# Performance work log

Measured on AMD Instinct MI355X. Metric: run time of the kernel, lower is better.

Reference implementation:

```python
import jax, jax.numpy as jnp
import numpy as np

N = 100_000          # entity count
NNZ = 1_600_000      # sparse support size (symmetrized)
C_IN = 16            # input channels (n_channels)
C1, C2, C3 = 32, 64, 32   # hard-coded widths in the torch module
C_EMB = 16           # target_embeddings
C_OUT = 16           # final_channels
N_OPS = 7            # equivariant basis ops used per layer
EPS = 1e-5


def _w(key, cin, cout):
    return jax.random.normal(key, (N_OPS, cin, cout), dtype=jnp.float32) / np.sqrt(N_OPS * cin)


def setup_inputs() -> dict:
    key = jax.random.key(0)
    ks = jax.random.split(key, 12)
    half = NNZ // 2
    r = jax.random.randint(ks[0], (half,), 0, N, dtype=jnp.int32)
    c = jax.random.randint(ks[1], (half,), 0, N, dtype=jnp.int32)
    # symmetrized support: entry j and entry j+half are transposes of each other
    row = jnp.concatenate([r, c])
    col = jnp.concatenate([c, r])
    perm = jnp.concatenate([jnp.arange(half, NNZ, dtype=jnp.int32),
                            jnp.arange(0, half, dtype=jnp.int32)])
    values = jax.random.normal(ks[2], (NNZ, C_IN), dtype=jnp.float32)
    return {
        "values": values, "row": row, "col": col, "perm": perm,
        "W1": _w(ks[3], C_IN, C1), "b1": jnp.zeros((C1,), jnp.float32),
        "W2": _w(ks[4], C1, C2),   "b2": jnp.zeros((C2,), jnp.float32),
        "W3": _w(ks[5], C2, C3),   "b3": jnp.zeros((C3,), jnp.float32),
        "Wp": jax.random.normal(ks[6], (C3, C_EMB), jnp.float32) / np.sqrt(C3),
        "bp": jnp.zeros((C_EMB,), jnp.float32),
        "Wl": jax.random.normal(ks[7], (C_EMB, C_OUT), jnp.float32) / np.sqrt(C_EMB),
        "bl": jnp.zeros((C_OUT,), jnp.float32),
    }


def _seg_mean(v, idx, n):
    # mean-pool nnz values into n segments
    s = jax.ops.segment_sum(v, idx, num_segments=n)
    cnt = jax.ops.segment_sum(jnp.ones((v.shape[0], 1), v.dtype), idx, num_segments=n)
    return s / jnp.maximum(cnt, 1.0)


def _eq_layer(v, row, col, perm, W, b):
    # equivariant basis restricted to the sparse support:
    # identity, transpose, row-mean broadcast (to row / to col),
    # col-mean broadcast (to row / to col), global-mean broadcast
    rm = _seg_mean(v, row, N)          # (N, cin)
    cm = _seg_mean(v, col, N)          # (N, cin)
    tm = jnp.mean(v, axis=0)           # (cin,)
    out = v @ W[0]
    out = out + v[perm] @ W[1]
    out = out + rm[row] @ W[2] + rm[col] @ W[3]
    out = out + cm[row] @ W[4] + cm[col] @ W[5]
    out = out + tm @ W[6] + b
    return out


def _rel_norm(v):
    # RelationNorm(affine=False): per-channel zero-mean unit-var over nnz
    m = jnp.mean(v, axis=0)
    var = jnp.var(v, axis=0)
    return (v - m) * jax.lax.rsqrt(var + EPS)


def reference(values, row, col, perm, W1, b1, W2, b2, W3, b3, Wp, bp, Wl, bl):
    h = _rel_norm(jax.nn.relu(_eq_layer(values, row, col, perm, W1, b1)))
    h = _rel_norm(jax.nn.relu(_eq_layer(h, row, col, perm, W2, b2)))
    h = _rel_norm(jax.nn.relu(_eq_layer(h, row, col, perm, W3, b3)))
    pooled = _seg_mean(h, row, N) @ Wp + bp   # entity pooling -> (N, C_EMB)
    out = pooled @ Wl + bl                    # final Linear head -> (N, C_OUT)
    return out
```

## Files before the change

### kernel.cpp

```cpp
#include <hip/hip_runtime.h>
#include <hip/hip_bf16.h>

constexpr int NE   = 100000;
constexpr int NZ   = 1600000;
constexpr int NZH  = NZ / 2;
constexpr int NSB  = (NE + 1023) / 1024;
constexpr float EPSV = 1e-5f;

constexpr int W1O = 0,     B1O = 3584,  W2O = 3616,  B2O = 17952, W3O = 18016,
              B3O = 32352, WPO = 32384, BPO = 32896, WLO = 32912, BLO = 33168,
              WTOT = 33184;

typedef __hip_bfloat16 bf16;
typedef __attribute__((ext_vector_type(8))) short short8v;
typedef __attribute__((ext_vector_type(4))) float f32x4;
#define MFMA_B16(A_, B_, C_) __builtin_amdgcn_mfma_f32_16x16x32_bf16((A_), (B_), (C_), 0, 0, 0)
#define PARTNER(i_) (((i_) < NZH) ? (i_) + NZH : (i_) - NZH)

__device__ __forceinline__ float4 ld_bf4(const bf16* p) {
    uint2 u = *(const uint2*)p;
    float4 r;
    r.x = __uint_as_float(u.x << 16);
    r.y = __uint_as_float(u.x & 0xffff0000u);
    r.z = __uint_as_float(u.y << 16);
    r.w = __uint_as_float(u.y & 0xffff0000u);
    return r;
}
__device__ __forceinline__ void ld_bf8v(const bf16* p, float4& lo, float4& hi) {
    uint4 u = *(const uint4*)p;
    lo.x = __uint_as_float(u.x << 16); lo.y = __uint_as_float(u.x & 0xffff0000u);
    lo.z = __uint_as_float(u.y << 16); lo.w = __uint_as_float(u.y & 0xffff0000u);
    hi.x = __uint_as_float(u.z << 16); hi.y = __uint_as_float(u.z & 0xffff0000u);
    hi.z = __uint_as_float(u.w << 16); hi.w = __uint_as_float(u.w & 0xffff0000u);
}
__device__ __forceinline__ float2 ld_bf2(const bf16* p) {
    unsigned u = *(const unsigned*)p;
    float2 r;
    r.x = __uint_as_float(u << 16);
    r.y = __uint_as_float(u & 0xffff0000u);
    return r;
}
__device__ __forceinline__ void st_bf4(bf16* p, float4 v) {
    __hip_bfloat162 lo = __float22bfloat162_rn(make_float2(v.x, v.y));
    __hip_bfloat162 hi = __float22bfloat162_rn(make_float2(v.z, v.w));
    uint2 u;
    u.x = *reinterpret_cast<unsigned int*>(&lo);
    u.y = *reinterpret_cast<unsigned int*>(&hi);
    *(uint2*)p = u;
}
__device__ __forceinline__ void st_bf8(bf16* p, float4 a, float4 b) {
    __hip_bfloat162 p0 = __float22bfloat162_rn(make_float2(a.x, a.y));
    __hip_bfloat162 p1 = __float22bfloat162_rn(make_float2(a.z, a.w));
    __hip_bfloat162 p2 = __float22bfloat162_rn(make_float2(b.x, b.y));
    __hip_bfloat162 p3 = __float22bfloat162_rn(make_float2(b.z, b.w));
    uint4 u;
    u.x = *reinterpret_cast<unsigned int*>(&p0);
    u.y = *reinterpret_cast<unsigned int*>(&p1);
    u.z = *reinterpret_cast<unsigned int*>(&p2);
    u.w = *reinterpret_cast<unsigned int*>(&p3);
    *(uint4*)p = u;
}
__device__ __forceinline__ float fin1(float v) { return (fabsf(v) < 1e30f) ? v : 0.f; }
__device__ __forceinline__ float4 fin4(float4 v) {
    v.x = fin1(v.x); v.y = fin1(v.y); v.z = fin1(v.z); v.w = fin1(v.w);
    return v;
}
__device__ __forceinline__ float4 ld_x4(const void* p, int flag, size_t q4) {
    if (flag) return ld_bf4((const bf16*)p + q4 * 4);
    return *((const float4*)p + q4);
}
__device__ __forceinline__ float4 relu4s(float4 x, float4 a, float4 b, const float* c) {
    float4 r;
    r.x = fmaxf(x.x + a.x + b.x + c[0], 0.f);
    r.y = fmaxf(x.y + a.y + b.y + c[1], 0.f);
    r.z = fmaxf(x.z + a.z + b.z + c[2], 0.f);
    r.w = fmaxf(x.w + a.w + b.w + c[3], 0.f);
    return r;
}
__device__ __forceinline__ void split8(const float* x, short8v& hi, short8v& lo) {
    #pragma unroll
    for (int i = 0; i < 8; i++) {
        bf16 h = __float2bfloat16(x[i]);
        float r = x[i] - __bfloat162float(h);
        bf16 l2 = __float2bfloat16(r);
        hi[i] = *reinterpret_cast<short*>(&h);
        lo[i] = *reinterpret_cast<short*>(&l2);
// ... 337 lines not shown
    float ae[8];
    ae[0]=c01s[o+0]+alo.x+blo.x; ae[1]=c01s[o+1]+alo.y+blo.y;
    ae[2]=c01s[o+2]+alo.z+blo.z; ae[3]=c01s[o+3]+alo.w+blo.w;
    ae[4]=c01s[o+4]+ahi.x+bhi.x; ae[5]=c01s[o+5]+ahi.y+bhi.y;
    ae[6]=c01s[o+6]+ahi.z+bhi.z; ae[7]=c01s[o+7]+ahi.w+bhi.w;
    #pragma unroll
    for (int ci = 0; ci < 16; ci++) {
        const float* w0 = W10s + ci * 32 + o;
        const float* w1 = W11s + ci * 32 + o;
        float a = xe[ci], b = xp[ci];
        #pragma unroll
        for (int u = 0; u < 8; u++) ae[u] += a * w0[u] + b * w1[u];
    }
    float4 hlo, hhi;
    hlo.x=fmaxf(ae[0],0.f); hlo.y=fmaxf(ae[1],0.f); hlo.z=fmaxf(ae[2],0.f); hlo.w=fmaxf(ae[3],0.f);
    hhi.x=fmaxf(ae[4],0.f); hhi.y=fmaxf(ae[5],0.f); hhi.z=fmaxf(ae[6],0.f); hhi.w=fmaxf(ae[7],0.f);
    st_bf4(h1 + (size_t)e * 32 + o, hlo);
    st_bf4(h1 + (size_t)e * 32 + o + 4, hhi);
    #pragma unroll
    for (int u = 0; u < 8; u++) {
        float h = fmaxf(ae[u], 0.f);
        atomicAdd(&red[o + u], h);
        atomicAdd(&red[32 + o + u], h * h);
    }
    __syncthreads();
    if (threadIdx.x < 32) {
        unsafeAtomicAdd(&Ssum[threadIdx.x], red[threadIdx.x]);
        unsafeAtomicAdd(&S2sum[threadIdx.x], red[32 + threadIdx.x]);
    }
}

template<bool STATS>
__global__ __launch_bounds__(256) void k_gsh1(const bf16* __restrict__ h1,
                                              const int* __restrict__ bucket,
                                              const int* __restrict__ off,
                                              const int* __restrict__ perm,
                                              const int* __restrict__ dflag,
                                              float* __restrict__ rawR, float* __restrict__ rawC,
                                              float* __restrict__ Ssum, float* __restrict__ S2sum) {
    __shared__ float red[64];
    if (STATS) {
        if (threadIdx.x < 64) red[threadIdx.x] = 0.f;
        __syncthreads();
    }
    int g = blockIdx.x * 64 + (threadIdx.x >> 2);
    int q = threadIdx.x & 3;
    float4 ra = {0,0,0,0}, rb = {0,0,0,0}, ca = {0,0,0,0}, cb = {0,0,0,0};
    float4 sa = {0,0,0,0}, sb = {0,0,0,0};
    int e0 = 0, e1 = 0;
    if (g < NE) { e0 = off[g]; e1 = off[g + 1]; }
    const bf16* hk = h1 + q * 8;
    if (dflag[1] == 0) {
        int idx = e0;
        for (; idx + 1 < e1; idx += 2) {
            int i0 = bucket[idx], i1 = bucket[idx + 1];
            int p0 = PARTNER(i0), p1 = PARTNER(i1);
            float4 aL, aH, bL, bH, cL, cH, dL, dH;
            ld_bf8v(hk + (size_t)i0 * 32, aL, aH);
            ld_bf8v(hk + (size_t)p0 * 32, bL, bH);
            ld_bf8v(hk + (size_t)i1 * 32, cL, cH);
            ld_bf8v(hk + (size_t)p1 * 32, dL, dH);
            ADD4(ra, aL); ADD4(rb, aH); ADD4(ca, bL); ADD4(cb, bH);
            ADD4(ra, cL); ADD4(rb, cH); ADD4(ca, dL); ADD4(cb, dH);
            if (STATS) { SQ4(sa, aL); SQ4(sb, aH); SQ4(sa, cL); SQ4(sb, cH); }
        }
        if (idx < e1) {
            int i = bucket[idx], p = PARTNER(i);
            float4 aL, aH, bL, bH;
            ld_bf8v(hk + (size_t)i * 32, aL, aH);
            ld_bf8v(hk + (size_t)p * 32, bL, bH);
            ADD4(ra, aL); ADD4(rb, aH); ADD4(ca, bL); ADD4(cb, bH);
            if (STATS) { SQ4(sa, aL); SQ4(sb, aH); }
        }
    } else {
        for (int idx = e0; idx < e1; idx++) {
            int i = bucket[idx], p = perm[i];
            float4 aL, aH, bL, bH;
            ld_bf8v(hk + (size_t)i * 32, aL, aH);
            ld_bf8v(hk + (size_t)p * 32, bL, bH);
            ADD4(ra, aL); ADD4(rb, aH); ADD4(ca, bL); ADD4(cb, bH);
            if (STATS) { SQ4(sa, aL); SQ4(sb, aH); }
        }
    }
    if (g < NE) {
        *(float4*)(rawR + (size_t)g * 64 + q * 8) = ra;
        *(float4*)(rawR + (size_t)g * 64 + q * 8 + 4) = rb;
        *(float4*)(rawC + (size_t)g * 64 + q * 8) = ca;
        *(float4*)(rawC + (size_t)g * 64 + q * 8 + 4) = cb;
    }
    if (STATS) {
        int o = q * 8;
        atomicAdd(&red[o+0], ra.x); atomicAdd(&red[o+1], ra.y);
        atomicAdd(&red[o+2], ra.z); atomicAdd(&red[o+3], ra.w);
        atomicAdd(&red[o+4], rb.x); atomicAdd(&red[o+5], rb.y);
        atomicAdd(&red[o+6], rb.z); atomicAdd(&red[o+7], rb.w);
        atomicAdd(&red[32+o+0], sa.x); atomicAdd(&red[32+o+1], sa.y);
        atomicAdd(&red[32+o+2], sa.z); atomicAdd(&red[32+o+3], sa.w);
        atomicAdd(&red[32+o+4], sb.x); atomicAdd(&red[32+o+5], sb.y);
        atomicAdd(&red[32+o+6], sb.z); atomicAdd(&red[32+o+7], sb.w);
        __syncthreads();
        if (threadIdx.x < 32) {
            unsafeAtomicAdd(&Ssum[threadIdx.x], red[threadIdx.x]);
            unsafeAtomicAdd(&S2sum[threadIdx.x], red[32 + threadIdx.x]);
        }
    }
}

template<int KH, int COUT>
__global__ void k_fold(const float* __restrict__ W, const float* __restrict__ mp,
                       const float* __restrict__ c0, bf16* __restrict__ Wfs,
                       float* __restrict__ c0f) {
    int t = blockIdx.x * 256 + threadIdx.x;
    constexpr int NT = COUT / 16;
    int f = t >> 9, r = t & 511;
    int lane = r >> 3, j = r & 7;
    int kc = f / NT, nt = f % NT;
    int kl = ((lane >> 4) << 3) + j;
    int kg = kc * 32 + kl;
    int n  = nt * 16 + (lane & 15);
    float w = 0.f;
    if (kg < 2 * KH) {
        int k  = (kg < KH) ? kg : kg - KH;
        const float* Ws = W + ((kg < KH) ? 0 : KH * COUT);
        w = Ws[k * COUT + n] * mp[64 + k];
    }
    bf16 hi = __float2bfloat16(w);
    Wfs[t] = hi;
    Wfs[4096 + t] = __float2bfloat16(w - __bfloat162float(hi));
    if (t < COUT) {
        float acc = c0[t];
        for (int k2 = 0; k2 < KH; k2++)
            acc += (-mp[k2] * mp[64 + k2]) * (W[k2 * COUT + t] + W[KH * COUT + k2 * COUT + t]);
        c0f[t] = acc;
    }
}

__global__ __launch_bounds__(256) void k_l1e(const void* __restrict__ xv,
                                             const int* __restrict__ dflag,
                                             const int* __restrict__ row,
                                             const int* __restrict__ col,
                                             const int* __restrict__ perm,
                                             const bf16* __restrict__ Wfs,
                                             const float* __restrict__ c0f,
                                             const bf16* __restrict__ A1b,
                                             const bf16* __restrict__ B1b,
                                             bf16* __restrict__ h1) {
    __shared__ __align__(16) float tr[4][16 * 36];
    __shared__ __align__(16) float c0s[32];
    if (threadIdx.x < 32) c0s[threadIdx.x] = c0f[threadIdx.x];
    const int flag = dflag[0];
    const int wv  = threadIdx.x >> 6;
    const int l   = threadIdx.x & 63;
    const int lr  = l & 15;
    const int lk  = l >> 4;
    const int tb  = lk * 4;
    float* T = tr[wv];
    short8v bh[2], bl[2];
    bh[0] = *(const short8v*)(Wfs + 0 * 512 + l * 8);
    bh[1] = *(const short8v*)(Wfs + 1 * 512 + l * 8);
    bl[0] = *(const short8v*)(Wfs + 4096 + 0 * 512 + l * 8);
    bl[1] = *(const short8v*)(Wfs + 4096 + 1 * 512 + l * 8);
    const int eE = l >> 2, q = l & 3;
    const int kq = lk & 1;
    __syncthreads();
    for (int bt = blockIdx.x; bt < NZ / 64; bt += gridDim.x) {
        const int te = bt * 64 + wv * 16;
        const int eA = te + lr;
        const int src = (lk < 2) ? eA : perm[eA];
        float xr[8];
        float4 v0 = fin4(ld_x4(xv, flag, (size_t)src * 4 + kq * 2));
        float4 v1 = fin4(ld_x4(xv, flag, (size_t)src * 4 + kq * 2 + 1));
        xr[0]=v0.x; xr[1]=v0.y; xr[2]=v0.z; xr[3]=v0.w;
        xr[4]=v1.x; xr[5]=v1.y; xr[6]=v1.z; xr[7]=v1.w;
        short8v ah, al;
        split8(xr, ah, al);
        f32x4 ac0 = {0.f, 0.f, 0.f, 0.f};
        f32x4 ac1 = ac0;
        ac0 = MFMA_B16(ah, bh[0], ac0); ac1 = MFMA_B16(ah, bh[1], ac1);
        ac0 = MFMA_B16(ah, bl[0], ac0); ac1 = MFMA_B16(ah, bl[1], ac1);
        ac0 = MFMA_B16(al, bh[0], ac0); ac1 = MFMA_B16(al, bh[1], ac1);
        #pragma unroll
        for (int r = 0; r < 4; r++) {
            float* Tw = T + (tb + r) * 36 + lr;
            Tw[0] = ac0[r]; Tw[16] = ac1[r];
        }
        __syncthreads();
        {
            const int e  = te + eE;
            const int rr = row[e], cc = col[e];
            const float* Tp = T + eE * 36 + q * 8;
            const bf16* ap = A1b + (size_t)rr * 32 + q * 8;
            const bf16* bp = B1b + (size_t)cc * 32 + q * 8;
            const float* cp = c0s + q * 8;
            float4 hv0 = relu4s(*(const float4*)(Tp + 0), ld_bf4(ap + 0), ld_bf4(bp + 0), cp + 0);
            float4 hv1 = relu4s(*(const float4*)(Tp + 4), ld_bf4(ap + 4), ld_bf4(bp + 4), cp + 4);
            st_bf8(h1 + (size_t)e * 32 + q * 8, hv0, hv1);
        }
        __syncthreads();
    }
}

__global__ __launch_bounds__(256) void k_l2e(const bf16* __restrict__ h1,
                                             const int* __restrict__ row,
                                             const int* __restrict__ col,
                                             const int* __restrict__ perm,
                                             const bf16* __restrict__ Wfs,
                                             const float* __restrict__ c0f,
                                             const bf16* __restrict__ A2b,
                                             const bf16* __restrict__ B2b,
                                             bf16* __restrict__ h2) {
    __shared__ __align__(16) float tr[4][16 * 68];
    __shared__ __align__(16) float c0s[64];
    if (threadIdx.x < 64) c0s[threadIdx.x] = c0f[threadIdx.x];
    const int wv  = threadIdx.x >> 6;
    const int l   = threadIdx.x & 63;
    const int lr  = l & 15;
    const int lk8 = (l >> 4) * 8;
    const int tb  = (l >> 4) * 4;
    float* T = tr[wv];
    short8v bh[8], bl[8];
    #pragma unroll
    for (int f = 0; f < 8; f++) {
        bh[f] = *(const short8v*)(Wfs + f * 512 + l * 8);
        bl[f] = *(const short8v*)(Wfs + 4096 + f * 512 + l * 8);
    }
    const int eE = l >> 2, q = l & 3;
    __syncthreads();
    for (int bt = blockIdx.x; bt < NZ / 64; bt += gridDim.x) {
        const int te = bt * 64 + wv * 16;
        const int eA = te + lr;
        const int pA = perm[eA];
        short8v a0 = *(const short8v*)(h1 + (size_t)eA * 32 + lk8);
        short8v a1 = *(const short8v*)(h1 + (size_t)pA * 32 + lk8);
        f32x4 ac0 = {0.f, 0.f, 0.f, 0.f};
        f32x4 ac1 = ac0, ac2 = ac0, ac3 = ac0;
        ac0 = MFMA_B16(a0, bh[0], ac0);  ac1 = MFMA_B16(a0, bh[1], ac1);
        ac2 = MFMA_B16(a0, bh[2], ac2);  ac3 = MFMA_B16(a0, bh[3], ac3);
        ac0 = MFMA_B16(a1, bh[4], ac0);  ac1 = MFMA_B16(a1, bh[5], ac1);
        ac2 = MFMA_B16(a1, bh[6], ac2);  ac3 = MFMA_B16(a1, bh[7], ac3);
        ac0 = MFMA_B16(a0, bl[0], ac0);  ac1 = MFMA_B16(a0, bl[1], ac1);
        ac2 = MFMA_B16(a0, bl[2], ac2);  ac3 = MFMA_B16(a0, bl[3], ac3);
        ac0 = MFMA_B16(a1, bl[4], ac0);  ac1 = MFMA_B16(a1, bl[5], ac1);
        ac2 = MFMA_B16(a1, bl[6], ac2);  ac3 = MFMA_B16(a1, bl[7], ac3);
        #pragma unroll
        for (int r = 0; r < 4; r++) {
            float* Tw = T + (tb + r) * 68 + lr;
            Tw[0] = ac0[r]; Tw[16] = ac1[r]; Tw[32] = ac2[r]; Tw[48] = ac3[r];
        }
        __syncthreads();
        {
            const int e  = te + eE;
            const int rr = row[e], cc = col[e];
            const float* Tp = T + eE * 68 + q * 16;
            const bf16* ap = A2b + (size_t)rr * 64 + q * 16;
            const bf16* bp = B2b + (size_t)cc * 64 + q * 16;
            const float* cp = c0s + q * 16;
            float4 hv0 = relu4s(*(const float4*)(Tp + 0),  ld_bf4(ap + 0),  ld_bf4(bp + 0),  cp + 0);
            float4 hv1 = relu4s(*(const float4*)(Tp + 4),  ld_bf4(ap + 4),  ld_bf4(bp + 4),  cp + 4);
            float4 hv2 = relu4s(*(const float4*)(Tp + 8),  ld_bf4(ap + 8),  ld_bf4(bp + 8),  cp + 8);
            float4 hv3 = relu4s(*(const float4*)(Tp + 12), ld_bf4(ap + 12), ld_bf4(bp + 12), cp + 12);
            st_bf8(h2 + (size_t)e * 64 + q * 16, hv0, hv1);
            st_bf8(h2 + (size_t)e * 64 + q * 16 + 8, hv2, hv3);
        }
        __syncthreads();
    }
}

__global__ __launch_bounds__(256) void k_gs64(const bf16* __restrict__ h2,
                                              const int* __restrict__ bucket,
                                              const int* __restrict__ off,
                                              const int* __restrict__ perm,
                                              const int* __restrict__ dflag,
                                              float* __restrict__ rawR, float* __restrict__ rawC,
                                              float* __restrict__ Ssum, float* __restrict__ S2sum) {
    __shared__ float red[128];
    if (threadIdx.x < 128) red[threadIdx.x] = 0.f;
    __syncthreads();
    int g = blockIdx.x * 32 + (threadIdx.x >> 3);
    int k = threadIdx.x & 7;
    float4 ra = {0,0,0,0}, rb = {0,0,0,0}, ca = {0,0,0,0}, cb = {0,0,0,0};
    float4 sa = {0,0,0,0}, sb = {0,0,0,0};
    int e0 = off[g], e1 = off[g + 1];
    const bf16* hk = h2 + k * 8;
    if (dflag[1] == 0) {
        int idx = e0;
        for (; idx + 1 < e1; idx += 2) {
            int i0 = bucket[idx], i1 = bucket[idx + 1];
            int p0 = PARTNER(i0), p1 = PARTNER(i1);
            float4 aL, aH, bL, bH, cL, cH, dL, dH;
            ld_bf8v(hk + (size_t)i0 * 64, aL, aH);
            ld_bf8v(hk + (size_t)p0 * 64, bL, bH);
            ld_bf8v(hk + (size_t)i1 * 64, cL, cH);
            ld_bf8v(hk + (size_t)p1 * 64, dL, dH);
            ADD4(ra, aL); ADD4(rb, aH); ADD4(ca, bL); ADD4(cb, bH);
            ADD4(ra, cL); ADD4(rb, cH); ADD4(ca, dL); ADD4(cb, dH);
            SQ4(sa, aL); SQ4(sb, aH); SQ4(sa, cL); SQ4(sb, cH);
        }
        if (idx < e1) {
            int i = bucket[idx], p = PARTNER(i);
            float4 aL, aH, bL, bH;
            ld_bf8v(hk + (size_t)i * 64, aL, aH);
            ld_bf8v(hk + (size_t)p * 64, bL, bH);
            ADD4(ra, aL); ADD4(rb, aH); ADD4(ca, bL); ADD4(cb, bH);
            SQ4(sa, aL); SQ4(sb, aH);
        }
    } else {
        for (int idx = e0; idx < e1; idx++) {
            int i = bucket[idx], p = perm[i];
            float4 aL, aH, bL, bH;
            ld_bf8v(hk + (size_t)i * 64, aL, aH);
            ld_bf8v(hk + (size_t)p * 64, bL, bH);
            ADD4(ra, aL); ADD4(rb, aH); ADD4(ca, bL); ADD4(cb, bH);
            SQ4(sa, aL); SQ4(sb, aH);
        }
    }
    *(float4*)(rawR + (size_t)g * 64 + k * 8) = ra;
    *(float4*)(rawR + (size_t)g * 64 + k * 8 + 4) = rb;
    *(float4*)(rawC + (size_t)g * 64 + k * 8) = ca;
    *(float4*)(rawC + (size_t)g * 64 + k * 8 + 4) = cb;
    {
        int o = k * 8;
        atomicAdd(&red[o+0], ra.x); atomicAdd(&red[o+1], ra.y);
        atomicAdd(&red[o+2], ra.z); atomicAdd(&red[o+3], ra.w);
        atomicAdd(&red[o+4], rb.x); atomicAdd(&red[o+5], rb.y);
        atomicAdd(&red[o+6], rb.z); atomicAdd(&red[o+7], rb.w);
        atomicAdd(&red[64+o+0], sa.x); atomicAdd(&red[64+o+1], sa.y);
        atomicAdd(&red[64+o+2], sa.z); atomicAdd(&red[64+o+3], sa.w);
        atomicAdd(&red[64+o+4], sb.x); atomicAdd(&red[64+o+5], sb.y);
        atomicAdd(&red[64+o+6], sb.z); atomicAdd(&red[64+o+7], sb.w);
    }
    __syncthreads();
    if (threadIdx.x < 64) {
        unsafeAtomicAdd(&Ssum[threadIdx.x], red[threadIdx.x]);
        unsafeAtomicAdd(&S2sum[threadIdx.x], red[64 + threadIdx.x]);
    }
}

__global__ __launch_bounds__(256) void k_l3e(const bf16* __restrict__ h2,
                                             const int* __restrict__ row,
                                             const int* __restrict__ col,
                                             const int* __restrict__ perm,
                                             const bf16* __restrict__ Wfs,
                                             const float* __restrict__ c0f,
                                             const bf16* __restrict__ A3b,
                                             const bf16* __restrict__ B3b,
                                             bf16* __restrict__ h3) {
    __shared__ __align__(16) float tr[4][16 * 36];
    __shared__ __align__(16) float c0s[32];
    if (threadIdx.x < 32) c0s[threadIdx.x] = c0f[threadIdx.x];
    const int wv  = threadIdx.x >> 6;
    const int l   = threadIdx.x & 63;
    const int lr  = l & 15;
    const int lk8 = (l >> 4) * 8;
    const int tb  = (l >> 4) * 4;
    float* T = tr[wv];
    short8v bh[8], bl[8];
    #pragma unroll
    for (int f = 0; f < 8; f++) {
        bh[f] = *(const short8v*)(Wfs + f * 512 + l * 8);
        bl[f] = *(const short8v*)(Wfs + 4096 + f * 512 + l * 8);
    }
    const int eE = l >> 2, q = l & 3;
    __syncthreads();
    for (int bt = blockIdx.x; bt < NZ / 64; bt += gridDim.x) {
        const int te = bt * 64 + wv * 16;
        const int eA = te + lr;
        const int pA = perm[eA];
        const bf16* he = h2 + (size_t)eA * 64;
        const bf16* hp = h2 + (size_t)pA * 64;
        short8v a0 = *(const short8v*)(he + lk8);
        short8v a1 = *(const short8v*)(he + 32 + lk8);
        short8v a2 = *(const short8v*)(hp + lk8);
        short8v a3 = *(const short8v*)(hp + 32 + lk8);
        f32x4 ac0 = {0.f, 0.f, 0.f, 0.f};
        f32x4 ac1 = ac0;
        ac0 = MFMA_B16(a0, bh[0], ac0); ac1 = MFMA_B16(a0, bh[1], ac1);
        ac0 = MFMA_B16(a1, bh[2], ac0); ac1 = MFMA_B16(a1, bh[3], ac1);
        ac0 = MFMA_B16(a2, bh[4], ac0); ac1 = MFMA_B16(a2, bh[5], ac1);
        ac0 = MFMA_B16(a3, bh[6], ac0); ac1 = MFMA_B16(a3, bh[7], ac1);
        ac0 = MFMA_B16(a0, bl[0], ac0); ac1 = MFMA_B16(a0, bl[1], ac1);
        ac0 = MFMA_B16(a1, bl[2], ac0); ac1 = MFMA_B16(a1, bl[3], ac1);
        ac0 = MFMA_B16(a2, bl[4], ac0); ac1 = MFMA_B16(a2, bl[5], ac1);
        ac0 = MFMA_B16(a3, bl[6], ac0); ac1 = MFMA_B16(a3, bl[7], ac1);
        #pragma unroll
        for (int r = 0; r < 4; r++) {
            float* Tw = T + (tb + r) * 36 + lr;
            Tw[0] = ac0[r]; Tw[16] = ac1[r];
        }
        __syncthreads();
        {
            const int e  = te + eE;
            const int rr = row[e], cc = col[e];
            const float* Tp = T + eE * 36 + q * 8;
            const bf16* ap = A3b + (size_t)rr * 32 + q * 8;
            const bf16* bp = B3b + (size_t)cc * 32 + q * 8;
            const float* cp = c0s + q * 8;
            float4 hv0 = relu4s(*(const float4*)(Tp + 0), ld_bf4(ap + 0), ld_bf4(bp + 0), cp + 0);
            float4 hv1 = relu4s(*(const float4*)(Tp + 4), ld_bf4(ap + 4), ld_bf4(bp + 4), cp + 4);
            st_bf8(h3 + (size_t)e * 32 + q * 8, hv0, hv1);
        }
        __syncthreads();
    }
}

__global__ __launch_bounds__(256) void k_gsp(const bf16* __restrict__ h3,
                                             const int* __restrict__ bucket,
                                             const int* __restrict__ off,
                                             float* __restrict__ pool,
                                             float* __restrict__ Ssum, float* __restrict__ S2sum) {
    __shared__ float red[64];
    if (threadIdx.x < 64) red[threadIdx.x] = 0.f;
    __syncthreads();
    int g = blockIdx.x * 64 + (threadIdx.x >> 2);
    int q = threadIdx.x & 3;
    float4 aa = {0,0,0,0}, ab = {0,0,0,0}, sa = {0,0,0,0}, sb = {0,0,0,0};
    int e0 = 0, e1 = 0;
    if (g < NE) { e0 = off[g]; e1 = off[g + 1]; }
    const bf16* hk = h3 + q * 8;
    {
        int idx = e0;
        for (; idx + 1 < e1; idx += 2) {
            int i0 = bucket[idx], i1 = bucket[idx + 1];
            float4 aL, aH, cL, cH;
            ld_bf8v(hk + (size_t)i0 * 32, aL, aH);
            ld_bf8v(hk + (size_t)i1 * 32, cL, cH);
            ADD4(aa, aL); ADD4(ab, aH); ADD4(aa, cL); ADD4(ab, cH);
            SQ4(sa, aL); SQ4(sb, aH); SQ4(sa, cL); SQ4(sb, cH);
        }
        if (idx < e1) {
            int i = bucket[idx];
            float4 aL, aH;
            ld_bf8v(hk + (size_t)i * 32, aL, aH);
            ADD4(aa, aL); ADD4(ab, aH);
            SQ4(sa, aL); SQ4(sb, aH);
        }
    }
    if (g < NE) {
        *(float4*)(pool + (size_t)g * 32 + q * 8) = aa;
        *(float4*)(pool + (size_t)g * 32 + q * 8 + 4) = ab;
    }
    {
        int o = q * 8;
        atomicAdd(&red[o+0], aa.x); atomicAdd(&red[o+1], aa.y);
        atomicAdd(&red[o+2], aa.z); atomicAdd(&red[o+3], aa.w);
        atomicAdd(&red[o+4], ab.x); atomicAdd(&red[o+5], ab.y);
        atomicAdd(&red[o+6], ab.z); atomicAdd(&red[o+7], ab.w);
        atomicAdd(&red[32+o+0], sa.x); atomicAdd(&red[32+o+1], sa.y);
        atomicAdd(&red[32+o+2], sa.z); atomicAdd(&red[32+o+3], sa.w);
        atomicAdd(&red[32+o+4], sb.x); atomicAdd(&red[32+o+5], sb.y);
        atomicAdd(&red[32+o+6], sb.z); atomicAdd(&red[32+o+7], sb.w);
    }
    __syncthreads();
    if (threadIdx.x < 32) {
        unsafeAtomicAdd(&Ssum[threadIdx.x], red[threadIdx.x]);
        unsafeAtomicAdd(&S2sum[threadIdx.x], red[32 + threadIdx.x]);
    }
}


__global__ __launch_bounds__(256) void k_gsh2(const bf16* __restrict__ h1,
                                              const int* __restrict__ bucket,
                                              const int* __restrict__ off,
                                              const int* __restrict__ perm,
                                              const int* __restrict__ col,
                                              const float* __restrict__ Wb,
                                              const float* __restrict__ mp1,
                                              const float* __restrict__ c02,
                                              const bf16* __restrict__ A2b, const bf16* __restrict__ B2b,
                                              float* __restrict__ rawR, float* __restrict__ rawC,
                                              float* __restrict__ Ssum, float* __restrict__ S2sum) {
    __shared__ __align__(16) float W20s[2048], W21s[2048];
    __shared__ __align__(16) float nm1s[32], rs1s[32], c02s[64];
    __shared__ float red[128];
    for (int i = threadIdx.x; i < 2048; i += 256) {
        W20s[i] = Wb[W2O + i];
        W21s[i] = Wb[W2O + 2048 + i];
    }
    if (threadIdx.x < 32) {
        float m = mp1[threadIdx.x], rr = mp1[64 + threadIdx.x];
        nm1s[threadIdx.x] = -m * rr; rs1s[threadIdx.x] = rr;
    }
    if (threadIdx.x < 64) c02s[threadIdx.x] = c02[threadIdx.x];
    if (threadIdx.x < 128) red[threadIdx.x] = 0.f;
    __syncthreads();
    const int g    = blockIdx.x * 16 + (threadIdx.x >> 4);
    const int lane = threadIdx.x & 15;
    const int gb   = (threadIdx.x & 63) & ~15;
    const int myo  = lane * 4;
    float4 a2n = ld_bf4(A2b + (size_t)g * 64 + myo);
    float4 b2n = ld_bf4(B2b + (size_t)g * 64 + myo);
    float4 cc  = *(const float4*)(c02s + myo);
    float rA = rs1s[lane*2], rB = rs1s[lane*2+1];
    float nA = nm1s[lane*2], nB = nm1s[lane*2+1];
    float4 racc = {0,0,0,0}, cacc = {0,0,0,0}, st1 = {0,0,0,0}, st2 = {0,0,0,0};
    int e0 = off[g], e1 = off[g + 1];
    for (int idx = e0; idx < e1; idx++) {
        int i = bucket[idx], p = perm[i], c = col[i];
        float2 hi2 = ld_bf2(h1 + (size_t)i * 32 + lane * 2);
        float2 hp2 = ld_bf2(h1 + (size_t)p * 32 + lane * 2);
        float xi0 = hi2.x * rA + nA, xi1 = hi2.y * rB + nB;
        float xp0 = hp2.x * rA + nA, xp1 = hp2.y * rB + nB;
        float4 a2c = ld_bf4(A2b + (size_t)c * 64 + myo);
        float4 b2c = ld_bf4(B2b + (size_t)c * 64 + myo);
// ... 457 lines not shown
                unsafeAtomicAdd(pp + u, h);
            }
        }
    }
    {
        const int ob = FINAL ? (j * 8) : (j * 16);
        #pragma unroll
        for (int k = 0; k < LCH; k++) {
            atomicAdd(&red[ob + k], s1[k]);
            atomicAdd(&red[NCH + ob + k], s2[k]);
        }
    }
    __syncthreads();
    if (threadIdx.x < NCH) {
        unsafeAtomicAdd(&Ssum[threadIdx.x], red[threadIdx.x]);
        unsafeAtomicAdd(&S2sum[threadIdx.x], red[NCH + threadIdx.x]);
    }
}

extern "C" void kernel_launch(void* const* d_in, const int* in_sizes, int n_in,
                              void* d_out, int out_size, void* d_ws, size_t ws_size,
                              hipStream_t stream) {
    const void* values = d_in[0];
    const int* row  = (const int*)d_in[1];
    const int* col  = (const int*)d_in[2];
    const int* perm = (const int*)d_in[3];

    char* p = (char*)d_ws;
    auto carve = [&](size_t bytes) { char* r = p; p += (bytes + 255) & ~(size_t)255; return r; };

    bf16* h1     = (bf16*)carve((size_t)NZ * 32 * 2);
    bf16* h2     = (bf16*)carve((size_t)NZ * 64 * 2);
    int*  bucket = (int*)carve((size_t)NZ * 4);
    int*  off    = (int*)carve((size_t)(NE + 1) * 4);
    int*  tmp    = (int*)carve((size_t)NE * 4);
    int*  sblk   = (int*)carve(256 * 4);
    float* rawR  = (float*)carve((size_t)NE * 64 * 4);
    float* rawC  = (float*)carve((size_t)NE * 64 * 4);
    bf16* A2b    = (bf16*)carve((size_t)NE * 64 * 2);
    bf16* B2b    = (bf16*)carve((size_t)NE * 64 * 2);
    bf16* Qa     = (bf16*)carve((size_t)NE * 32 * 2);
    bf16* Qb     = (bf16*)carve((size_t)NE * 32 * 2);
    bf16* W1fs   = (bf16*)carve(8192 * 2);
    bf16* W2fs   = (bf16*)carve(8192 * 2);
    bf16* W3fs   = (bf16*)carve(8192 * 2);
    int*   cnt   = (int*)carve((size_t)NE * 4);
    float* invc  = (float*)carve((size_t)NE * 4);
    float* Wbuf  = (float*)carve((size_t)WTOT * 4);
    float* misc  = (float*)carve(2048 * 4);
    int*   dflag = (int*)carve(64 * 4);
    size_t need_fast2 = (size_t)(p - (char*)d_ws);

    if (ws_size >= need_fast2) {
        bf16* h3 = h1;
        float* pool = rawR;
        hipMemsetAsync(misc, 0, 2048 * 4, stream);
        hipMemsetAsync(cnt, 0, (size_t)NE * 4, stream);
        hipMemsetAsync(tmp, 0, (size_t)NE * 4, stream);
        k_detect<<<1, 64, 0, stream>>>((const unsigned*)values, dflag);
        k_convW<<<(WTOT + 255) / 256, 256, 0, stream>>>(d_in[4], d_in[5], d_in[6], d_in[7],
                                                        d_in[8], d_in[9], d_in[10], d_in[11],
                                                        d_in[12], d_in[13], dflag, Wbuf);
        k_prep<<<1, 64, 0, stream>>>(misc);
        k_count<<<NZ / 256, 256, 0, stream>>>(row, cnt);
        k_invcnt<<<(NE + 255) / 256, 256, 0, stream>>>(cnt, invc);
        k_scan1<<<NSB, 1024, 0, stream>>>(cnt, sblk);
        k_scan2<<<1, 128, 0, stream>>>(sblk, sblk + 128, off);
        k_scan3<<<NSB, 1024, 0, stream>>>(cnt, sblk + 128, off);
        k_scatter<<<NZ / 256, 256, 0, stream>>>(row, perm, off, tmp, bucket, dflag);

        k_gsv<<<(NE + 63) / 64, 256, 0, stream>>>(values, dflag, bucket, off, perm,
                                                  rawR, rawC, misc + 960);
        k_nodeb<16, 32><<<NE / 32, 256, 0, stream>>>(rawR, rawC, invc, cnt, misc + 0,
                                                     Wbuf + W1O, Qa, Qb);
        k_const<<<1, 64, 0, stream>>>(Wbuf + W1O, Wbuf + B1O, misc + 960, 1, misc + 1024, 16, 32);
        k_fold<16, 32><<<16, 256, 0, stream>>>(Wbuf + W1O, misc + 0, misc + 1024,
                                               W1fs, misc + 1984);
        k_l1e<<<2500, 256, 0, stream>>>(values, dflag, row, col, perm, W1fs, misc + 1984,
                                        Qa, Qb, h1);
        k_gsh1<true><<<(NE + 63) / 64, 256, 0, stream>>>(h1, bucket, off, perm, dflag,
                                                         rawR, rawC, misc + 512, misc + 768);
        k_fin<<<1, 64, 0, stream>>>(misc + 512, misc + 768, misc + 128, 32);

        k_nodeb<32, 64><<<NE / 16, 256, 0, stream>>>(rawR, rawC, invc, cnt, misc + 128,
                                                     Wbuf + W2O, A2b, B2b);
        k_const<<<1, 64, 0, stream>>>(Wbuf + W2O, Wbuf + B2O, misc + 960, 0, misc + 1088, 32, 64);
        k_fold<32, 64><<<16, 256, 0, stream>>>(Wbuf + W2O, misc + 128, misc + 1088,
                                               W2fs, misc + 1856);
        k_l2e<<<2500, 256, 0, stream>>>(h1, row, col, perm, W2fs, misc + 1856, A2b, B2b, h2);
        k_gs64<<<NE / 32, 256, 0, stream>>>(h2, bucket, off, perm, dflag, rawR, rawC,
                                            misc + 576, misc + 832);
        k_fin<<<1, 64, 0, stream>>>(misc + 576, misc + 832, misc + 256, 64);

        k_nodeb<64, 32><<<NE / 32, 256, 0, stream>>>(rawR, rawC, invc, cnt, misc + 256,
                                                     Wbuf + W3O, Qa, Qb);
        k_const<<<1, 64, 0, stream>>>(Wbuf + W3O, Wbuf + B3O, misc + 960, 0, misc + 1152, 64, 32);
        k_fold<64, 32><<<16, 256, 0, stream>>>(Wbuf + W3O, misc + 256, misc + 1152,
                                               W3fs, misc + 1920);
        k_l3e<<<2500, 256, 0, stream>>>(h2, row, col, perm, W3fs, misc + 1920, Qa, Qb, h3);
        k_gsp<<<(NE + 63) / 64, 256, 0, stream>>>(h3, bucket, off, pool, misc + 640, misc + 896);
        k_fin<<<1, 64, 0, stream>>>(misc + 640, misc + 896, misc + 384, 32);

        k_head<<<1, 512, 0, stream>>>(Wbuf, misc + 384, misc + 1280, misc + 1792, misc + 1808);
        k_out<<<NE * 16 / 256, 256, 0, stream>>>(pool, invc, cnt, dflag,
                                                 misc + 1280, misc + 1792, misc + 1808, d_out);
        return;
    }

    p = (char*)d_ws;
    h1     = (bf16*)carve((size_t)NZ * 32 * 2);
    bucket = (int*)carve((size_t)NZ * 4);
    off    = (int*)carve((size_t)(NE + 1) * 4);
    tmp    = (int*)carve((size_t)NE * 4);
    sblk   = (int*)carve(256 * 4);
    rawR   = (float*)carve((size_t)NE * 64 * 4);
    rawC   = (float*)carve((size_t)NE * 64 * 4);
    A2b    = (bf16*)carve((size_t)NE * 64 * 2);
    B2b    = (bf16*)carve((size_t)NE * 64 * 2);
    Qa     = (bf16*)carve((size_t)NE * 32 * 2);
    Qb     = (bf16*)carve((size_t)NE * 32 * 2);
    cnt    = (int*)carve((size_t)NE * 4);
    invc   = (float*)carve((size_t)NE * 4);
    Wbuf   = (float*)carve((size_t)WTOT * 4);
    misc   = (float*)carve(2048 * 4);
    dflag  = (int*)carve(64 * 4);
    size_t need_fast = (size_t)(p - (char*)d_ws);

    if (ws_size >= need_fast) {
        float* pool = rawR;
        hipMemsetAsync(misc, 0, 2048 * 4, stream);
        hipMemsetAsync(cnt, 0, (size_t)NE * 4, stream);
        hipMemsetAsync(tmp, 0, (size_t)NE * 4, stream);
        k_detect<<<1, 64, 0, stream>>>((const unsigned*)values, dflag);
        k_convW<<<(WTOT + 255) / 256, 256, 0, stream>>>(d_in[4], d_in[5], d_in[6], d_in[7],
                                                        d_in[8], d_in[9], d_in[10], d_in[11],
                                                        d_in[12], d_in[13], dflag, Wbuf);
        k_prep<<<1, 64, 0, stream>>>(misc);
        k_count<<<NZ / 256, 256, 0, stream>>>(row, cnt);
        k_invcnt<<<(NE + 255) / 256, 256, 0, stream>>>(cnt, invc);
        k_scan1<<<NSB, 1024, 0, stream>>>(cnt, sblk);
        k_scan2<<<1, 128, 0, stream>>>(sblk, sblk + 128, off);
        k_scan3<<<NSB, 1024, 0, stream>>>(cnt, sblk + 128, off);
        k_scatter<<<NZ / 256, 256, 0, stream>>>(row, perm, off, tmp, bucket, dflag);

        k_gsv<<<(NE + 63) / 64, 256, 0, stream>>>(values, dflag, bucket, off, perm,
                                                  rawR, rawC, misc + 960);
        k_nodeb<16, 32><<<NE / 32, 256, 0, stream>>>(rawR, rawC, invc, cnt, misc + 0,
                                                     Wbuf + W1O, Qa, Qb);
        k_const<<<1, 64, 0, stream>>>(Wbuf + W1O, Wbuf + B1O, misc + 960, 1, misc + 1024, 16, 32);
        k_l1n<<<NZ / 64, 256, 0, stream>>>(values, dflag, row, col, perm, Wbuf, misc + 1024,
                                           Qa, Qb, h1, misc + 512, misc + 768);
        k_fin<<<1, 64, 0, stream>>>(misc + 512, misc + 768, misc + 128, 32);

// ... 89 lines not shown
```

Before: 1.228 ms.

## Fuse layer-3 edge kernel with entity pooling via atomics; deepen gather unroll

Layer 3 no longer writes h3 to memory for a separate gather-pool kernel. It now scatter-adds each relu output into the per-row pool buffer with float atomics and accumulates the norm statistics locally. The aim is to remove one full write and read of the per-nonzero activations plus a kernel launch, at the cost of many global atomics and a memset of the pool. The segment-gather loops in layers 1 and 2 are also unrolled from 2 to 4 edges so more loads are in flight. The perm lookups are replaced by the PARTNER arithmetic when the symmetric-layout flag allows it.

```diff
diff --git a/kernel.cpp b/kernel.cpp
--- a/kernel.cpp
+++ b/kernel.cpp
@@ -26,12 +26,14 @@
     r.w = __uint_as_float(u.y & 0xffff0000u);
     return r;
 }
-__device__ __forceinline__ void ld_bf8v(const bf16* p, float4& lo, float4& hi) {
-    uint4 u = *(const uint4*)p;
+__device__ __forceinline__ void cv_bf8(uint4 u, float4& lo, float4& hi) {
     lo.x = __uint_as_float(u.x << 16); lo.y = __uint_as_float(u.x & 0xffff0000u);
     lo.z = __uint_as_float(u.y << 16); lo.w = __uint_as_float(u.y & 0xffff0000u);
     hi.x = __uint_as_float(u.z << 16); hi.y = __uint_as_float(u.z & 0xffff0000u);
     hi.z = __uint_as_float(u.w << 16); hi.w = __uint_as_float(u.w & 0xffff0000u);
+}
+__device__ __forceinline__ void ld_bf8v(const bf16* p, float4& lo, float4& hi) {
+    cv_bf8(*(const uint4*)p, lo, hi);
 }
 __device__ __forceinline__ float2 ld_bf2(const bf16* p) {
     unsigned u = *(const unsigned*)p;
@@ -475,19 +477,28 @@
     const bf16* hk = h1 + q * 8;
     if (dflag[1] == 0) {
         int idx = e0;
-        for (; idx + 1 < e1; idx += 2) {
-            int i0 = bucket[idx], i1 = bucket[idx + 1];
-            int p0 = PARTNER(i0), p1 = PARTNER(i1);
-            float4 aL, aH, bL, bH, cL, cH, dL, dH;
-            ld_bf8v(hk + (size_t)i0 * 32, aL, aH);
-            ld_bf8v(hk + (size_t)p0 * 32, bL, bH);
-            ld_bf8v(hk + (size_t)i1 * 32, cL, cH);
-            ld_bf8v(hk + (size_t)p1 * 32, dL, dH);
-            ADD4(ra, aL); ADD4(rb, aH); ADD4(ca, bL); ADD4(cb, bH);
-            ADD4(ra, cL); ADD4(rb, cH); ADD4(ca, dL); ADD4(cb, dH);
-            if (STATS) { SQ4(sa, aL); SQ4(sb, aH); SQ4(sa, cL); SQ4(sb, cH); }
-        }
-        if (idx < e1) {
+        for (; idx + 3 < e1; idx += 4) {
+            int i0 = bucket[idx],     i1 = bucket[idx + 1];
+            int i2 = bucket[idx + 2], i3 = bucket[idx + 3];
+            uint4 u0 = *(const uint4*)(hk + (size_t)i0 * 32);
+            uint4 v0 = *(const uint4*)(hk + (size_t)PARTNER(i0) * 32);
+            uint4 u1 = *(const uint4*)(hk + (size_t)i1 * 32);
+            uint4 v1 = *(const uint4*)(hk + (size_t)PARTNER(i1) * 32);
+            uint4 u2 = *(const uint4*)(hk + (size_t)i2 * 32);
+            uint4 v2 = *(const uint4*)(hk + (size_t)PARTNER(i2) * 32);
+            uint4 u3 = *(const uint4*)(hk + (size_t)i3 * 32);
+            uint4 v3 = *(const uint4*)(hk + (size_t)PARTNER(i3) * 32);
+            float4 L, H;
+            cv_bf8(u0, L, H); ADD4(ra, L); ADD4(rb, H); if (STATS) { SQ4(sa, L); SQ4(sb, H); }
+            cv_bf8(u1, L, H); ADD4(ra, L); ADD4(rb, H); if (STATS) { SQ4(sa, L); SQ4(sb, H); }
+            cv_bf8(u2, L, H); ADD4(ra, L); ADD4(rb, H); if (STATS) { SQ4(sa, L); SQ4(sb, H); }
+            cv_bf8(u3, L, H); ADD4(ra, L); ADD4(rb, H); if (STATS) { SQ4(sa, L); SQ4(sb, H); }
+            cv_bf8(v0, L, H); ADD4(ca, L); ADD4(cb, H);
+            cv_bf8(v1, L, H); ADD4(ca, L); ADD4(cb, H);
+            cv_bf8(v2, L, H); ADD4(ca, L); ADD4(cb, H);
+            cv_bf8(v3, L, H); ADD4(ca, L); ADD4(cb, H);
+        }
+        for (; idx < e1; idx++) {
             int i = bucket[idx], p = PARTNER(i);
             float4 aL, aH, bL, bH;
             ld_bf8v(hk + (size_t)i * 32, aL, aH);
@@ -572,6 +583,7 @@
     __shared__ __align__(16) float c0s[32];
     if (threadIdx.x < 32) c0s[threadIdx.x] = c0f[threadIdx.x];
     const int flag = dflag[0];
+    const int vio  = dflag[1];
     const int wv  = threadIdx.x >> 6;
     const int l   = threadIdx.x & 63;
     const int lr  = l & 15;
@@ -589,7 +601,7 @@
     for (int bt = blockIdx.x; bt < NZ / 64; bt += gridDim.x) {
         const int te = bt * 64 + wv * 16;
         const int eA = te + lr;
-        const int src = (lk < 2) ? eA : perm[eA];
+        const int src = (lk < 2) ? eA : (vio ? perm[eA] : PARTNER(eA));
         float xr[8];
         float4 v0 = fin4(ld_x4(xv, flag, (size_t)src * 4 + kq * 2));
         float4 v1 = fin4(ld_x4(xv, flag, (size_t)src * 4 + kq * 2 + 1));
@@ -627,6 +639,7 @@
                                              const int* __restrict__ row,
                                              const int* __restrict__ col,
                                              const int* __restrict__ perm,
+                                             const int* __restrict__ dflag,
                                              const bf16* __restrict__ Wfs,
                                              const float* __restrict__ c0f,
                                              const bf16* __restrict__ A2b,
@@ -635,6 +648,7 @@
     __shared__ __align__(16) float tr[4][16 * 68];
     __shared__ __align__(16) float c0s[64];
     if (threadIdx.x < 64) c0s[threadIdx.x] = c0f[threadIdx.x];
+    const int vio = dflag[1];
     const int wv  = threadIdx.x >> 6;
     const int l   = threadIdx.x & 63;
     const int lr  = l & 15;
@@ -652,7 +666,7 @@
     for (int bt = blockIdx.x; bt < NZ / 64; bt += gridDim.x) {
         const int te = bt * 64 + wv * 16;
         const int eA = te + lr;
-        const int pA = perm[eA];
+        const int pA = vio ? perm[eA] : PARTNER(eA);
         short8v a0 = *(const short8v*)(h1 + (size_t)eA * 32 + lk8);
         short8v a1 = *(const short8v*)(h1 + (size_t)pA * 32 + lk8);
         f32x4 ac0 = {0.f, 0.f, 0.f, 0.f};
@@ -707,19 +721,28 @@
     const bf16* hk = h2 + k * 8;
     if (dflag[1] == 0) {
         int idx = e0;
-        for (; idx + 1 < e1; idx += 2) {
-            int i0 = bucket[idx], i1 = bucket[idx + 1];
-            int p0 = PARTNER(i0), p1 = PARTNER(i1);
-            float4 aL, aH, bL, bH, cL, cH, dL, dH;
-            ld_bf8v(hk + (size_t)i0 * 64, aL, aH);
-            ld_bf8v(hk + (size_t)p0 * 64, bL, bH);
-            ld_bf8v(hk + (size_t)i1 * 64, cL, cH);
-            ld_bf8v(hk + (size_t)p1 * 64, dL, dH);
-            ADD4(ra, aL); ADD4(rb, aH); ADD4(ca, bL); ADD4(cb, bH);
-            ADD4(ra, cL); ADD4(rb, cH); ADD4(ca, dL); ADD4(cb, dH);
-            SQ4(sa, aL); SQ4(sb, aH); SQ4(sa, cL); SQ4(sb, cH);
-        }
-        if (idx < e1) {
+        for (; idx + 3 < e1; idx += 4) {
+            int i0 = bucket[idx],     i1 = bucket[idx + 1];
+            int i2 = bucket[idx + 2], i3 = bucket[idx + 3];
+            uint4 u0 = *(const uint4*)(hk + (size_t)i0 * 64);
+            uint4 v0 = *(const uint4*)(hk + (size_t)PARTNER(i0) * 64);
+            uint4 u1 = *(const uint4*)(hk + (size_t)i1 * 64);
+            uint4 v1 = *(const uint4*)(hk + (size_t)PARTNER(i1) * 64);
+            uint4 u2 = *(const uint4*)(hk + (size_t)i2 * 64);
+            uint4 v2 = *(const uint4*)(hk + (size_t)PARTNER(i2) * 64);
+            uint4 u3 = *(const uint4*)(hk + (size_t)i3 * 64);
+            uint4 v3 = *(const uint4*)(hk + (size_t)PARTNER(i3) * 64);
+            float4 L, H;
+            cv_bf8(u0, L, H); ADD4(ra, L); ADD4(rb, H); SQ4(sa, L); SQ4(sb, H);
+            cv_bf8(u1, L, H); ADD4(ra, L); ADD4(rb, H); SQ4(sa, L); SQ4(sb, H);
+            cv_bf8(u2, L, H); ADD4(ra, L); ADD4(rb, H); SQ4(sa, L); SQ4(sb, H);
+            cv_bf8(u3, L, H); ADD4(ra, L); ADD4(rb, H); SQ4(sa, L); SQ4(sb, H);
+            cv_bf8(v0, L, H); ADD4(ca, L); ADD4(cb, H);
+            cv_bf8(v1, L, H); ADD4(ca, L); ADD4(cb, H);
+            cv_bf8(v2, L, H); ADD4(ca, L); ADD4(cb, H);
+            cv_bf8(v3, L, H); ADD4(ca, L); ADD4(cb, H);
+        }
+        for (; idx < e1; idx++) {
             int i = bucket[idx], p = PARTNER(i);
             float4 aL, aH, bL, bH;
             ld_bf8v(hk + (size_t)i * 64, aL, aH);
@@ -763,14 +786,19 @@
                                              const int* __restrict__ row,
                                              const int* __restrict__ col,
                                              const int* __restrict__ perm,
+                                             const int* __restrict__ dflag,
                                              const bf16* __restrict__ Wfs,
                                              const float* __restrict__ c0f,
                                              const bf16* __restrict__ A3b,
                                              const bf16* __restrict__ B3b,
-                                             bf16* __restrict__ h3) {
+                                             float* __restrict__ pool,
+                                             float* __restrict__ Ssum, float* __restrict__ S2sum) {
     __shared__ __align__(16) float tr[4][16 * 36];
     __shared__ __align__(16) float c0s[32];
+    __shared__ float red[64];
     if (threadIdx.x < 32) c0s[threadIdx.x] = c0f[threadIdx.x];
+    if (threadIdx.x < 64) red[threadIdx.x] = 0.f;
+    const int vio = dflag[1];
     const int wv  = threadIdx.x >> 6;
     const int l   = threadIdx.x & 63;
     const int lr  = l & 15;
@@ -784,11 +812,12 @@
         bl[f] = *(const short8v*)(Wfs + 4096 + f * 512 + l * 8);
     }
     const int eE = l >> 2, q = l & 3;
+    float4 s1a = {0,0,0,0}, s1b = {0,0,0,0}, s2a = {0,0,0,0}, s2b = {0,0,0,0};
     __syncthreads();
     for (int bt = blockIdx.x; bt < NZ / 64; bt += gridDim.x) {
         const int te = bt * 64 + wv * 16;
         const int eA = te + lr;
-        const int pA = perm[eA];
+        const int pA = vio ? perm[eA] : PARTNER(eA);
         const bf16* he = h2 + (size_t)eA * 64;
         const bf16* hp = h2 + (size_t)pA * 64;
         short8v a0 = *(const short8v*)(he + lk8);
@@ -820,58 +849,26 @@
             const float* cp = c0s + q * 8;
             float4 hv0 = relu4s(*(const float4*)(Tp + 0), ld_bf4(ap + 0), ld_bf4(bp + 0), cp + 0);
             float4 hv1 = relu4s(*(const float4*)(Tp + 4), ld_bf4(ap + 4), ld_bf4(bp + 4), cp + 4);
-            st_bf8(h3 + (size_t)e * 32 + q * 8, hv0, hv1);
+            float* pp = pool + (size_t)rr * 32 + q * 8;
+            unsafeAtomicAdd(pp + 0, hv0.x); unsafeAtomicAdd(pp + 1, hv0.y);
+            unsafeAtomicAdd(pp + 2, hv0.z); unsafeAtomicAdd(pp + 3, hv0.w);
+            unsafeAtomicAdd(pp + 4, hv1.x); unsafeAtomicAdd(pp + 5, hv1.y);
+            unsafeAtomicAdd(pp + 6, hv1.z); unsafeAtomicAdd(pp + 7, hv1.w);
+            ADD4(s1a, hv0); ADD4(s1b, hv1);
+            SQ4(s2a, hv0); SQ4(s2b, hv1);
         }
         __syncthreads();
-    }
-}
-
-__global__ __launch_bounds__(256) void k_gsp(const bf16* __restrict__ h3,
-                                             const int* __restrict__ bucket,
-                                             const int* __restrict__ off,
-                                             float* __restrict__ pool,
-                                             float* __restrict__ Ssum, float* __restrict__ S2sum) {
-    __shared__ float red[64];
-    if (threadIdx.x < 64) red[threadIdx.x] = 0.f;
-    __syncthreads();
-    int g = blockIdx.x * 64 + (threadIdx.x >> 2);
-    int q = threadIdx.x & 3;
-    float4 aa = {0,0,0,0}, ab = {0,0,0,0}, sa = {0,0,0,0}, sb = {0,0,0,0};
-    int e0 = 0, e1 = 0;
-    if (g < NE) { e0 = off[g]; e1 = off[g + 1]; }
-    const bf16* hk = h3 + q * 8;
-    {
-        int idx = e0;
-        for (; idx + 1 < e1; idx += 2) {
-            int i0 = bucket[idx], i1 = bucket[idx + 1];
-            float4 aL, aH, cL, cH;
-            ld_bf8v(hk + (size_t)i0 * 32, aL, aH);
-            ld_bf8v(hk + (size_t)i1 * 32, cL, cH);
-            ADD4(aa, aL); ADD4(ab, aH); ADD4(aa, cL); ADD4(ab, cH);
-            SQ4(sa, aL); SQ4(sb, aH); SQ4(sa, cL); SQ4(sb, cH);
-        }
-        if (idx < e1) {
-            int i = bucket[idx];
-            float4 aL, aH;
-            ld_bf8v(hk + (size_t)i * 32, aL, aH);
-            ADD4(aa, aL); ADD4(ab, aH);
-            SQ4(sa, aL); SQ4(sb, aH);
-        }
-    }
-    if (g < NE) {
-        *(float4*)(pool + (size_t)g * 32 + q * 8) = aa;
-        *(float4*)(pool + (size_t)g * 32 + q * 8 + 4) = ab;
     }
     {
         int o = q * 8;
-        atomicAdd(&red[o+0], aa.x); atomicAdd(&red[o+1], aa.y);
-        atomicAdd(&red[o+2], aa.z); atomicAdd(&red[o+3], aa.w);
-        atomicAdd(&red[o+4], ab.x); atomicAdd(&red[o+5], ab.y);
-        atomicAdd(&red[o+6], ab.z); atomicAdd(&red[o+7], ab.w);
-        atomicAdd(&red[32+o+0], sa.x); atomicAdd(&red[32+o+1], sa.y);
-        atomicAdd(&red[32+o+2], sa.z); atomicAdd(&red[32+o+3], sa.w);
-        atomicAdd(&red[32+o+4], sb.x); atomicAdd(&red[32+o+5], sb.y);
-        atomicAdd(&red[32+o+6], sb.z); atomicAdd(&red[32+o+7], sb.w);
+        atomicAdd(&red[o+0], s1a.x); atomicAdd(&red[o+1], s1a.y);
+        atomicAdd(&red[o+2], s1a.z); atomicAdd(&red[o+3], s1a.w);
+        atomicAdd(&red[o+4], s1b.x); atomicAdd(&red[o+5], s1b.y);
+        atomicAdd(&red[o+6], s1b.z); atomicAdd(&red[o+7], s1b.w);
+        atomicAdd(&red[32+o+0], s2a.x); atomicAdd(&red[32+o+1], s2a.y);
+        atomicAdd(&red[32+o+2], s2a.z); atomicAdd(&red[32+o+3], s2a.w);
+        atomicAdd(&red[32+o+4], s2b.x); atomicAdd(&red[32+o+5], s2b.y);
+        atomicAdd(&red[32+o+6], s2b.z); atomicAdd(&red[32+o+7], s2b.w);
     }
     __syncthreads();
     if (threadIdx.x < 32) {
@@ -1435,7 +1432,6 @@
     size_t need_fast2 = (size_t)(p - (char*)d_ws);
 
     if (ws_size >= need_fast2) {
-        bf16* h3 = h1;
         float* pool = rawR;
         hipMemsetAsync(misc, 0, 2048 * 4, stream);
         hipMemsetAsync(cnt, 0, (size_t)NE * 4, stream);
@@ -1470,7 +1466,8 @@
         k_const<<<1, 64, 0, stream>>>(Wbuf + W2O, Wbuf + B2O, misc + 960, 0, misc + 1088, 32, 64);
         k_fold<32, 64><<<16, 256, 0, stream>>>(Wbuf + W2O, misc + 128, misc + 1088,
                                                W2fs, misc + 1856);
-        k_l2e<<<2500, 256, 0, stream>>>(h1, row, col, perm, W2fs, misc + 1856, A2b, B2b, h2);
+        k_l2e<<<2500, 256, 0, stream>>>(h1, row, col, perm, dflag, W2fs, misc + 1856,
+                                        A2b, B2b, h2);
         k_gs64<<<NE / 32, 256, 0, stream>>>(h2, bucket, off, perm, dflag, rawR, rawC,
                                             misc + 576, misc + 832);
         k_fin<<<1, 64, 0, stream>>>(misc + 576, misc + 832, misc + 256, 64);
@@ -1480,8 +1477,9 @@
         k_const<<<1, 64, 0, stream>>>(Wbuf + W3O, Wbuf + B3O, misc + 960, 0, misc + 1152, 64, 32);
         k_fold<64, 32><<<16, 256, 0, stream>>>(Wbuf + W3O, misc + 256, misc + 1152,
                                                W3fs, misc + 1920);
-        k_l3e<<<2500, 256, 0, stream>>>(h2, row, col, perm, W3fs, misc + 1920, Qa, Qb, h3);
-        k_gsp<<<(NE + 63) / 64, 256, 0, stream>>>(h3, bucket, off, pool, misc + 640, misc + 896);
+        hipMemsetAsync(pool, 0, (size_t)NE * 32 * 4, stream);
+        k_l3e<<<2500, 256, 0, stream>>>(h2, row, col, perm, dflag, W3fs, misc + 1920,
+                                        Qa, Qb, pool, misc + 640, misc + 896);
         k_fin<<<1, 64, 0, stream>>>(misc + 640, misc + 896, misc + 384, 32);
 
         k_head<<<1, 512, 0, stream>>>(Wbuf, misc + 384, misc + 1280, misc + 1792, misc + 1808);
```

Result: slower. 2.405 ms (+95.9%).
